# Kernel optimization log

Measured on AMD Instinct MI355X. Metric: run time of the kernel, lower is better.

The kernel has to match this reference:

```python
import jax, jax.numpy as jnp
import numpy as np

N_EMBD = 1024
N_HEAD = 16
D_HEAD = N_EMBD // N_HEAD
B, T = 4, 2048


def _layernorm(x, g, b, eps=1e-5):
    mu = jnp.mean(x, axis=-1, keepdims=True)
    var = jnp.var(x, axis=-1, keepdims=True)
    return (x - mu) * jax.lax.rsqrt(var + eps) * g + b


def setup_inputs() -> dict:
    key = jax.random.key(0)
    ks = jax.random.split(key, 16)
    C = N_EMBD
    s = 0.02
    return {
        "x": jax.random.normal(ks[0], (B, T, C), jnp.float32),
        "ln1_g": jnp.ones((C,), jnp.float32),
        "ln1_b": jnp.zeros((C,), jnp.float32),
        "Wq": jax.random.normal(ks[1], (C, C), jnp.float32) * s,
        "bq": jnp.zeros((C,), jnp.float32),
        "Wk": jax.random.normal(ks[2], (C, C), jnp.float32) * s,
        "bk": jnp.zeros((C,), jnp.float32),
        "Wv": jax.random.normal(ks[3], (C, C), jnp.float32) * s,
        "bv": jnp.zeros((C,), jnp.float32),
        "Wo": jax.random.normal(ks[4], (C, C), jnp.float32) * s,
        "bo": jnp.zeros((C,), jnp.float32),
        "ln2_g": jnp.ones((C,), jnp.float32),
        "ln2_b": jnp.zeros((C,), jnp.float32),
        "W1": jax.random.normal(ks[5], (C, 4 * C), jnp.float32) * s,
        "b1": jnp.zeros((4 * C,), jnp.float32),
        "W2": jax.random.normal(ks[6], (4 * C, C), jnp.float32) * s,
        "b2": jnp.zeros((C,), jnp.float32),
    }


def reference(x, ln1_g, ln1_b, Wq, bq, Wk, bk, Wv, bv, Wo, bo,
              ln2_g, ln2_b, W1, b1, W2, b2):
    Bx, Tx, C = x.shape
    H, D = N_HEAD, D_HEAD

    # --- attention (pre-LN) ---
    h = _layernorm(x, ln1_g, ln1_b)
    q = (h @ Wq + bq).reshape(Bx, Tx, H, D)
    k = (h @ Wk + bk).reshape(Bx, Tx, H, D)
    v = (h @ Wv + bv).reshape(Bx, Tx, H, D)
    att = jnp.einsum("bqhd,bkhd->bhqk", q, k) * (1.0 / jnp.sqrt(jnp.float32(D)))
    causal = jnp.tril(jnp.ones((Tx, Tx), bool))
    att = jnp.where(causal, att, -jnp.inf)
    att = jax.nn.softmax(att, axis=-1)
    y = jnp.einsum("bhqk,bkhd->bqhd", att, v).reshape(Bx, Tx, C)
    x = x + (y @ Wo + bo)

    # --- MLP (pre-LN), exact GELU as in torch F.gelu default ---
    h2 = _layernorm(x, ln2_g, ln2_b)
    m = jax.nn.gelu(h2 @ W1 + b1, approximate=False)
    x = x + (m @ W2 + b2)
    return x
```

## Files before the change

### kernel.cpp

```cpp
#include <hip/hip_runtime.h>
#include <hip/hip_bf16.h>
#include <math.h>

#define C_EMBD 1024
#define T_SEQ  2048
#define BATCH  4
#define NHEAD  16
#define DHEAD  64

typedef __attribute__((ext_vector_type(8))) short bf16x8;
typedef __attribute__((ext_vector_type(4))) float floatx4;

static __device__ __forceinline__ floatx4 mfma16(bf16x8 a, bf16x8 b, floatx4 c) {
    return __builtin_amdgcn_mfma_f32_16x16x32_bf16(a, b, c, 0, 0, 0);
}

static __device__ __forceinline__ void gl2lds16(const void* g, void* l) {
    __builtin_amdgcn_global_load_lds(
        (const __attribute__((address_space(1))) void*)g,
        (__attribute__((address_space(3))) void*)l, 16, 0, 0);
}

__global__ __launch_bounds__(256) void transpose_cvt(
        const float* __restrict__ W, __hip_bfloat16* __restrict__ Wt, int K, int N) {
    __shared__ float tile[32][33];
    const int tid = threadIdx.x;
    const int n0 = blockIdx.x * 32, k0 = blockIdx.y * 32;
    const int r = tid >> 3, c4 = (tid & 7) * 4;
    float4 v = *(const float4*)&W[(size_t)(k0 + r) * N + n0 + c4];
    tile[r][c4 + 0] = v.x; tile[r][c4 + 1] = v.y;
    tile[r][c4 + 2] = v.z; tile[r][c4 + 3] = v.w;
    __syncthreads();
    __align__(8) __hip_bfloat16 ob[4];
    ob[0] = __float2bfloat16(tile[c4 + 0][r]);
    ob[1] = __float2bfloat16(tile[c4 + 1][r]);
    ob[2] = __float2bfloat16(tile[c4 + 2][r]);
    ob[3] = __float2bfloat16(tile[c4 + 3][r]);
    *(short4*)&Wt[(size_t)(n0 + r) * K + k0 + c4] = *(short4*)ob;
}

__global__ __launch_bounds__(256) void ln_bf16(
        const float* __restrict__ x, const float* __restrict__ g,
        const float* __restrict__ b, __hip_bfloat16* __restrict__ out) {
    const int row = blockIdx.x, tid = threadIdx.x;
    const float4 v = ((const float4*)(x + (size_t)row * C_EMBD))[tid];
    float s  = v.x + v.y + v.z + v.w;
    float sq = v.x * v.x + v.y * v.y + v.z * v.z + v.w * v.w;
    #pragma unroll
    for (int off = 1; off < 64; off <<= 1) {
        s  += __shfl_xor(s, off);
        sq += __shfl_xor(sq, off);
    }
    __shared__ float ps[4], pq[4];
    if ((tid & 63) == 0) { ps[tid >> 6] = s; pq[tid >> 6] = sq; }
    __syncthreads();
    s  = ps[0] + ps[1] + ps[2] + ps[3];
    sq = pq[0] + pq[1] + pq[2] + pq[3];
    const float mu   = s * (1.0f / C_EMBD);
    const float var  = sq * (1.0f / C_EMBD) - mu * mu;
    const float rstd = rsqrtf(var + 1e-5f);
    const float4 gv = ((const float4*)g)[tid];
    const float4 bv = ((const float4*)b)[tid];
    __align__(8) __hip_bfloat16 ob[4];
    ob[0] = __float2bfloat16((v.x - mu) * rstd * gv.x + bv.x);
    ob[1] = __float2bfloat16((v.y - mu) * rstd * gv.y + bv.y);
    ob[2] = __float2bfloat16((v.z - mu) * rstd * gv.z + bv.z);
    ob[3] = __float2bfloat16((v.w - mu) * rstd * gv.w + bv.w);
    *(short4*)&out[(size_t)row * C_EMBD + tid * 4] = *(short4*)ob;
}

template <int EP>
__global__ __launch_bounds__(256, 2) void gemm_bt(
        const __hip_bfloat16* __restrict__ A, const __hip_bfloat16* __restrict__ Bt,
        int M, int N, int K,
        const float* __restrict__ ba, const float* __restrict__ bb, const float* __restrict__ bc,
        __hip_bfloat16* __restrict__ o0, __hip_bfloat16* __restrict__ o1,
        __hip_bfloat16* __restrict__ o2, float* __restrict__ of,
        const float* __restrict__ resid) {
    __shared__ __align__(16) __hip_bfloat16 As[128 * 32];
    __shared__ __align__(16) __hip_bfloat16 Bs[128 * 32];
    const int tid  = threadIdx.x;
    const int n0   = blockIdx.x * 128;
    const int m0   = blockIdx.y * 128;
    const int wave = tid >> 6, lane = tid & 63;
    const int l15  = lane & 15, quad = lane >> 4;
    const int wm   = (wave & 1) * 64, wn = (wave >> 1) * 64;
    const int c0   = wave * 2;
    const int sr   = lane >> 2;
    const int sc   = (lane & 3) * 8;

    const floatx4 z4 = {0.f, 0.f, 0.f, 0.f};
    floatx4 acc[4][4];
    #pragma unroll
    for (int i = 0; i < 4; i++)
        #pragma unroll
        for (int j = 0; j < 4; j++) acc[i][j] = z4;

    for (int k0 = 0; k0 < K; k0 += 32) {
        __syncthreads();
        gl2lds16(&A[(m0 + c0 * 16 + sr) * K + k0 + sc],       &As[c0 * 512]);
        gl2lds16(&A[(m0 + (c0 + 1) * 16 + sr) * K + k0 + sc], &As[(c0 + 1) * 512]);
        gl2lds16(&Bt[(n0 + c0 * 16 + sr) * K + k0 + sc],      &Bs[c0 * 512]);
        gl2lds16(&Bt[(n0 + (c0 + 1) * 16 + sr) * K + k0 + sc],&Bs[(c0 + 1) * 512]);
        __syncthreads();
        bf16x8 af[4], bfr[4];
        #pragma unroll
        for (int i = 0; i < 4; i++)
            af[i] = *(const bf16x8*)&As[(wm + i * 16 + l15) * 32 + quad * 8];
        #pragma unroll
        for (int j = 0; j < 4; j++)
            bfr[j] = *(const bf16x8*)&Bs[(wn + j * 16 + l15) * 32 + quad * 8];
        #pragma unroll
        for (int i = 0; i < 4; i++)
            #pragma unroll
            for (int j = 0; j < 4; j++)
                acc[i][j] = mfma16(af[i], bfr[j], acc[i][j]);
    }

    #pragma unroll
    for (int i = 0; i < 4; i++) {
        #pragma unroll
        for (int j = 0; j < 4; j++) {
            const int col = n0 + wn + j * 16 + l15;
            #pragma unroll
            for (int r = 0; r < 4; r++) {
                const int m = m0 + wm + i * 16 + quad * 4 + r;
                float val = acc[i][j][r];
                if (EP == 0) {
                    const int which = col >> 10, cn = col & 1023;
                    const float* bp = (which == 0) ? ba : (which == 1) ? bb : bc;
                    val += bp[cn];
                    const int head = cn >> 6, d = cn & 63;
                    const int bidx = m >> 11, t = m & 2047;
                    if (which == 0) {
                        val *= 0.125f;
                        o0[((bidx * NHEAD + head) * T_SEQ + t) * DHEAD + d] = __float2bfloat16(val);
                    } else if (which == 1) {
                        o1[((bidx * NHEAD + head) * T_SEQ + t) * DHEAD + d] = __float2bfloat16(val);
                    } else {
                        o2[((bidx * NHEAD + head) * DHEAD + d) * T_SEQ + t] = __float2bfloat16(val);
                    }
                } else if (EP == 1) {
                    val += ba[col];
                    of[m * N + col] = resid[m * N + col] + val;
                } else if (EP == 2) {
                    val += ba[col];
                    const float gl = 0.5f * val * (1.0f + erff(val * 0.70710678118654752f));
                    o0[m * N + col] = __float2bfloat16(gl);
                } else {
                    val += ba[col];
                    of[m * N + col] += val;
                }
            }
        }
    }
}

__global__ __launch_bounds__(256, 4) void attn_fa(
        const __hip_bfloat16* __restrict__ q, const __hip_bfloat16* __restrict__ k,
        const __hip_bfloat16* __restrict__ vt, __hip_bfloat16* __restrict__ y) {
    __shared__ __align__(16) __hip_bfloat16 pl[4][32 * 72];
    const int bh = blockIdx.y;
    const int tid = threadIdx.x;
    const int wave = tid >> 6, lane = tid & 63;
    const int l15 = lane & 15, quad = lane >> 4;
    const __hip_bfloat16* qp = q + (size_t)bh * T_SEQ * DHEAD;
    const __hip_bfloat16* kp = k + (size_t)bh * T_SEQ * DHEAD;
    const __hip_bfloat16* vp = vt + (size_t)bh * DHEAD * T_SEQ;
    const int chunk = (wave < 2) ? blockIdx.x : (31 - blockIdx.x);
    const int qw = chunk * 64 + (wave & 1) * 32;

    bf16x8 bq[2][2];
    #pragma unroll
    for (int qi = 0; qi < 2; qi++)
        #pragma unroll
        for (int h = 0; h < 2; h++)
            bq[qi][h] = *(const bf16x8*)&qp[(qw + qi * 16 + l15) * DHEAD + h * 32 + quad * 8];

    const floatx4 z4 = {0.f, 0.f, 0.f, 0.f};
    floatx4 oac[2][4];
    #pragma unroll
    for (int qi = 0; qi < 2; qi++)
        #pragma unroll
        for (int nd = 0; nd < 4; nd++) oac[qi][nd] = z4;
    float li[2] = {0.f, 0.f};

    __hip_bfloat16* myp = &pl[wave][0];

    auto body = [&](int kb, bool diag) {
        bf16x8 kf[4][2];
        #pragma unroll
        for (int nt = 0; nt < 4; nt++)
            #pragma unroll
            for (int h = 0; h < 2; h++)
                kf[nt][h] = *(const bf16x8*)&kp[(kb + nt * 16 + l15) * DHEAD + h * 32 + quad * 8];
        floatx4 sa[2][4];
        #pragma unroll
        for (int qi = 0; qi < 2; qi++)
            #pragma unroll
            for (int nt = 0; nt < 4; nt++) sa[qi][nt] = z4;
        #pragma unroll
        for (int nt = 0; nt < 4; nt++)
            #pragma unroll
            for (int h = 0; h < 2; h++) {
                sa[0][nt] = mfma16(kf[nt][h], bq[0][h], sa[0][nt]);
                sa[1][nt] = mfma16(kf[nt][h], bq[1][h], sa[1][nt]);
            }
        if (diag) {
            #pragma unroll
            for (int qi = 0; qi < 2; qi++)
                #pragma unroll
                for (int nt = 0; nt < 4; nt++)
                    #pragma unroll
                    for (int r = 0; r < 4; r++)
                        if (kb + nt * 16 + quad * 4 + r > qw + qi * 16 + l15)
                            sa[qi][nt][r] = -INFINITY;
        }
        #pragma unroll
        for (int qi = 0; qi < 2; qi++) {
            float sm = 0.f;
            #pragma unroll
            for (int nt = 0; nt < 4; nt++) {
                __align__(8) __hip_bfloat16 pk[4];
                #pragma unroll
                for (int r = 0; r < 4; r++) {
                    const float p = __expf(sa[qi][nt][r]);
                    sm += p;
                    pk[r] = __float2bfloat16(p);
                }
                *(short4*)&myp[(qi * 16 + l15) * 72 + nt * 16 + quad * 4] = *(short4*)pk;
            }
            li[qi] += sm;
        }
        asm volatile("" ::: "memory");
        bf16x8 vf[4][2];
        #pragma unroll
        for (int nd = 0; nd < 4; nd++)
            #pragma unroll
            for (int kh = 0; kh < 2; kh++)
                vf[nd][kh] = *(const bf16x8*)&vp[(nd * 16 + l15) * T_SEQ + kb + kh * 32 + quad * 8];
        asm volatile("s_waitcnt lgkmcnt(0)" ::: "memory");
        bf16x8 pf[2][2];
        #pragma unroll
        for (int qi = 0; qi < 2; qi++)
            #pragma unroll
            for (int kh = 0; kh < 2; kh++)
                pf[qi][kh] = *(const bf16x8*)&myp[(qi * 16 + l15) * 72 + kh * 32 + quad * 8];
        #pragma unroll
        for (int nd = 0; nd < 4; nd++)
            #pragma unroll
            for (int kh = 0; kh < 2; kh++) {
                oac[0][nd] = mfma16(vf[nd][kh], pf[0][kh], oac[0][nd]);
                oac[1][nd] = mfma16(vf[nd][kh], pf[1][kh], oac[1][nd]);
            }
    };

    const int nfull = chunk;
    for (int t = 0; t < nfull; t++) body(t * 64, false);
    body(nfull * 64, true);

    float inv[2];
    #pragma unroll
    for (int qi = 0; qi < 2; qi++) {
        float l = li[qi];
        l += __shfl_xor(l, 16);
        l += __shfl_xor(l, 32);
        inv[qi] = 1.0f / l;
    }
    #pragma unroll
    for (int qi = 0; qi < 2; qi++)
        #pragma unroll
        for (int nd = 0; nd < 4; nd++) {
            __align__(8) __hip_bfloat16 ok[4];
            #pragma unroll
            for (int r = 0; r < 4; r++) ok[r] = __float2bfloat16(oac[qi][nd][r] * inv[qi]);
            *(short4*)&myp[(qi * 16 + l15) * 72 + nd * 16 + quad * 4] = *(short4*)ok;
        }
    asm volatile("s_waitcnt lgkmcnt(0)" ::: "memory");
    const int b = bh >> 4, head = bh & 15;
    #pragma unroll
    for (int half = 0; half < 2; half++) {
        const int row = half * 16 + (lane >> 2);
        const int cb  = (lane & 3) * 16;
        const bf16x8 v0 = *(const bf16x8*)&myp[row * 72 + cb];
        const bf16x8 v1 = *(const bf16x8*)&myp[row * 72 + cb + 8];
        __hip_bfloat16* yr = &y[(size_t)(b * T_SEQ + qw + row) * C_EMBD + head * DHEAD + cb];
        *(bf16x8*)yr       = v0;
        *(bf16x8*)(yr + 8) = v1;
    }
}

extern "C" void kernel_launch(void* const* d_in, const int* in_sizes, int n_in,
                              void* d_out, int out_size, void* d_ws, size_t ws_size,
                              hipStream_t stream) {
    const float* x     = (const float*)d_in[0];
    const float* ln1_g = (const float*)d_in[1];
    const float* ln1_b = (const float*)d_in[2];
    const float* Wq    = (const float*)d_in[3];
    const float* bq    = (const float*)d_in[4];
    const float* Wk    = (const float*)d_in[5];
    const float* bk    = (const float*)d_in[6];
    const float* Wv    = (const float*)d_in[7];
    const float* bv    = (const float*)d_in[8];
    const float* Wo    = (const float*)d_in[9];
    const float* bo    = (const float*)d_in[10];
    const float* ln2_g = (const float*)d_in[11];
    const float* ln2_b = (const float*)d_in[12];
    const float* W1    = (const float*)d_in[13];
    const float* b1    = (const float*)d_in[14];
    const float* W2    = (const float*)d_in[15];
    const float* b2    = (const float*)d_in[16];
    float* out = (float*)d_out;

    char* ws = (char*)d_ws;
    __hip_bfloat16* wqkvt = (__hip_bfloat16*)(ws);
    __hip_bfloat16* wot   = (__hip_bfloat16*)(ws + 6291456);
    __hip_bfloat16* w1t   = (__hip_bfloat16*)(ws + 8388608);
    __hip_bfloat16* w2t   = (__hip_bfloat16*)(ws + 16777216);
    __hip_bfloat16* hbuf  = (__hip_bfloat16*)(ws + 25165824);
    __hip_bfloat16* qbuf  = (__hip_bfloat16*)(ws + 41943040);
    __hip_bfloat16* kbuf  = (__hip_bfloat16*)(ws + 58720256);
    __hip_bfloat16* vbuf  = (__hip_bfloat16*)(ws + 75497472);
    __hip_bfloat16* ybuf  = (__hip_bfloat16*)(ws + 92274688);
    __hip_bfloat16* mbuf  = (__hip_bfloat16*)(ws + 41943040);

    transpose_cvt<<<dim3(32, 32), 256, 0, stream>>>(Wq, wqkvt, 1024, 1024);
    transpose_cvt<<<dim3(32, 32), 256, 0, stream>>>(Wk, wqkvt + 1024 * 1024, 1024, 1024);
    transpose_cvt<<<dim3(32, 32), 256, 0, stream>>>(Wv, wqkvt + 2048 * 1024, 1024, 1024);
    transpose_cvt<<<dim3(32, 32), 256, 0, stream>>>(Wo, wot, 1024, 1024);
    transpose_cvt<<<dim3(128, 32), 256, 0, stream>>>(W1, w1t, 1024, 4096);
    transpose_cvt<<<dim3(32, 128), 256, 0, stream>>>(W2, w2t, 4096, 1024);

    ln_bf16<<<8192, 256, 0, stream>>>(x, ln1_g, ln1_b, hbuf);

    gemm_bt<0><<<dim3(24, 64), 256, 0, stream>>>(hbuf, wqkvt, 8192, 3072, 1024,
        bq, bk, bv, qbuf, kbuf, vbuf, nullptr, nullptr);

    attn_fa<<<dim3(16, 64), 256, 0, stream>>>(qbuf, kbuf, vbuf, ybuf);

    gemm_bt<1><<<dim3(8, 64), 256, 0, stream>>>(ybuf, wot, 8192, 1024, 1024,
        bo, nullptr, nullptr, nullptr, nullptr, nullptr, out, x);

    ln_bf16<<<8192, 256, 0, stream>>>(out, ln2_g, ln2_b, hbuf);

    gemm_bt<2><<<dim3(32, 64), 256, 0, stream>>>(hbuf, w1t, 8192, 4096, 1024,
        b1, nullptr, nullptr, mbuf, nullptr, nullptr, nullptr, nullptr);

    gemm_bt<3><<<dim3(8, 64), 256, 0, stream>>>(mbuf, w2t, 8192, 1024, 4096,
        b2, nullptr, nullptr, nullptr, nullptr, nullptr, out, nullptr);
}
```

Before: 610.6 us.

## Rebalance causal attention waves, remap blocks per XCD, and use exp2 softmax

Each wave now processes one 16-row query tile from a low chunk and one from the mirrored high chunk, so every wave in a block carries the same causal workload. The low-tile QK and PV MFMAs are skipped once past its diagonal. Blocks are linearly remapped so that the blocks on each XCD share the same batch-heads, aiming for better L2 reuse of K and V. The Q scale folds in log2(e) so the kernel can use the hardware exp2 instruction instead of __expf, and the extra branching adds some control overhead.

Measured after the change: 802.6 us. 1.31x slower.

```diff
diff --git a/kernel.cpp b/kernel.cpp
--- a/kernel.cpp
+++ b/kernel.cpp
@@ -10,6 +10,12 @@
 
 typedef __attribute__((ext_vector_type(8))) short bf16x8;
 typedef __attribute__((ext_vector_type(4))) float floatx4;
+
+#if __has_builtin(__builtin_amdgcn_exp2f)
+#define EXP2F __builtin_amdgcn_exp2f
+#else
+#define EXP2F exp2f
+#endif
 
 static __device__ __forceinline__ floatx4 mfma16(bf16x8 a, bf16x8 b, floatx4 c) {
     return __builtin_amdgcn_mfma_f32_16x16x32_bf16(a, b, c, 0, 0, 0);
@@ -133,7 +139,7 @@
                     const int head = cn >> 6, d = cn & 63;
                     const int bidx = m >> 11, t = m & 2047;
                     if (which == 0) {
-                        val *= 0.125f;
+                        val *= 0.18033688011112042f;
                         o0[((bidx * NHEAD + head) * T_SEQ + t) * DHEAD + d] = __float2bfloat16(val);
                     } else if (which == 1) {
                         o1[((bidx * NHEAD + head) * T_SEQ + t) * DHEAD + d] = __float2bfloat16(val);
@@ -160,22 +166,30 @@
         const __hip_bfloat16* __restrict__ q, const __hip_bfloat16* __restrict__ k,
         const __hip_bfloat16* __restrict__ vt, __hip_bfloat16* __restrict__ y) {
     __shared__ __align__(16) __hip_bfloat16 pl[4][32 * 72];
-    const int bh = blockIdx.y;
     const int tid = threadIdx.x;
     const int wave = tid >> 6, lane = tid & 63;
     const int l15 = lane & 15, quad = lane >> 4;
+
+    const int lin  = blockIdx.x + 16 * blockIdx.y;
+    const int xcd  = lin & 7;
+    const int slot = lin >> 3;
+    const int bh   = xcd * 8 + (slot >> 4);
+    const int c    = slot & 15;
+    const int hc   = 31 - c;
+
     const __hip_bfloat16* qp = q + (size_t)bh * T_SEQ * DHEAD;
     const __hip_bfloat16* kp = k + (size_t)bh * T_SEQ * DHEAD;
     const __hip_bfloat16* vp = vt + (size_t)bh * DHEAD * T_SEQ;
-    const int chunk = (wave < 2) ? blockIdx.x : (31 - blockIdx.x);
-    const int qw = chunk * 64 + (wave & 1) * 32;
+
+    const int qlo = c  * 64 + wave * 16;
+    const int qhi = hc * 64 + wave * 16;
 
     bf16x8 bq[2][2];
     #pragma unroll
-    for (int qi = 0; qi < 2; qi++)
-        #pragma unroll
-        for (int h = 0; h < 2; h++)
-            bq[qi][h] = *(const bf16x8*)&qp[(qw + qi * 16 + l15) * DHEAD + h * 32 + quad * 8];
+    for (int h = 0; h < 2; h++) {
+        bq[0][h] = *(const bf16x8*)&qp[(qlo + l15) * DHEAD + h * 32 + quad * 8];
+        bq[1][h] = *(const bf16x8*)&qp[(qhi + l15) * DHEAD + h * 32 + quad * 8];
+    }
 
     const floatx4 z4 = {0.f, 0.f, 0.f, 0.f};
     floatx4 oac[2][4];
@@ -187,7 +201,7 @@
 
     __hip_bfloat16* myp = &pl[wave][0];
 
-    auto body = [&](int kb, bool diag) {
+    auto body = [&](int kb, bool act0, bool m0, bool m1) {
         bf16x8 kf[4][2];
         #pragma unroll
         for (int nt = 0; nt < 4; nt++)
@@ -202,35 +216,60 @@
         #pragma unroll
         for (int nt = 0; nt < 4; nt++)
             #pragma unroll
-            for (int h = 0; h < 2; h++) {
-                sa[0][nt] = mfma16(kf[nt][h], bq[0][h], sa[0][nt]);
+            for (int h = 0; h < 2; h++)
                 sa[1][nt] = mfma16(kf[nt][h], bq[1][h], sa[1][nt]);
-            }
-        if (diag) {
-            #pragma unroll
-            for (int qi = 0; qi < 2; qi++)
-                #pragma unroll
-                for (int nt = 0; nt < 4; nt++)
-                    #pragma unroll
-                    for (int r = 0; r < 4; r++)
-                        if (kb + nt * 16 + quad * 4 + r > qw + qi * 16 + l15)
-                            sa[qi][nt][r] = -INFINITY;
-        }
-        #pragma unroll
-        for (int qi = 0; qi < 2; qi++) {
+        if (act0) {
+            #pragma unroll
+            for (int nt = 0; nt < 4; nt++)
+                #pragma unroll
+                for (int h = 0; h < 2; h++)
+                    sa[0][nt] = mfma16(kf[nt][h], bq[0][h], sa[0][nt]);
+        }
+        if (m1) {
+            #pragma unroll
+            for (int nt = 0; nt < 4; nt++)
+                #pragma unroll
+                for (int r = 0; r < 4; r++)
+                    if (kb + nt * 16 + quad * 4 + r > qhi + l15)
+                        sa[1][nt][r] = -INFINITY;
+        }
+        if (m0) {
+            #pragma unroll
+            for (int nt = 0; nt < 4; nt++)
+                #pragma unroll
+                for (int r = 0; r < 4; r++)
+                    if (kb + nt * 16 + quad * 4 + r > qlo + l15)
+                        sa[0][nt][r] = -INFINITY;
+        }
+        {
             float sm = 0.f;
             #pragma unroll
             for (int nt = 0; nt < 4; nt++) {
                 __align__(8) __hip_bfloat16 pk[4];
                 #pragma unroll
                 for (int r = 0; r < 4; r++) {
-                    const float p = __expf(sa[qi][nt][r]);
+                    const float p = EXP2F(sa[1][nt][r]);
                     sm += p;
                     pk[r] = __float2bfloat16(p);
                 }
-                *(short4*)&myp[(qi * 16 + l15) * 72 + nt * 16 + quad * 4] = *(short4*)pk;
+                *(short4*)&myp[(16 + l15) * 72 + nt * 16 + quad * 4] = *(short4*)pk;
             }
-            li[qi] += sm;
+            li[1] += sm;
+        }
+        if (act0) {
+            float sm = 0.f;
+            #pragma unroll
+            for (int nt = 0; nt < 4; nt++) {
+                __align__(8) __hip_bfloat16 pk[4];
+                #pragma unroll
+                for (int r = 0; r < 4; r++) {
+                    const float p = EXP2F(sa[0][nt][r]);
+                    sm += p;
+                    pk[r] = __float2bfloat16(p);
+                }
+                *(short4*)&myp[(l15) * 72 + nt * 16 + quad * 4] = *(short4*)pk;
+            }
+            li[0] += sm;
         }
         asm volatile("" ::: "memory");
         bf16x8 vf[4][2];
@@ -240,24 +279,33 @@
             for (int kh = 0; kh < 2; kh++)
                 vf[nd][kh] = *(const bf16x8*)&vp[(nd * 16 + l15) * T_SEQ + kb + kh * 32 + quad * 8];
         asm volatile("s_waitcnt lgkmcnt(0)" ::: "memory");
-        bf16x8 pf[2][2];
-        #pragma unroll
-        for (int qi = 0; qi < 2; qi++)
+        bf16x8 pf1[2];
+        #pragma unroll
+        for (int kh = 0; kh < 2; kh++)
+            pf1[kh] = *(const bf16x8*)&myp[(16 + l15) * 72 + kh * 32 + quad * 8];
+        if (act0) {
+            bf16x8 pf0[2];
             #pragma unroll
             for (int kh = 0; kh < 2; kh++)
-                pf[qi][kh] = *(const bf16x8*)&myp[(qi * 16 + l15) * 72 + kh * 32 + quad * 8];
-        #pragma unroll
-        for (int nd = 0; nd < 4; nd++)
-            #pragma unroll
-            for (int kh = 0; kh < 2; kh++) {
-                oac[0][nd] = mfma16(vf[nd][kh], pf[0][kh], oac[0][nd]);
-                oac[1][nd] = mfma16(vf[nd][kh], pf[1][kh], oac[1][nd]);
-            }
+                pf0[kh] = *(const bf16x8*)&myp[(l15) * 72 + kh * 32 + quad * 8];
+            #pragma unroll
+            for (int nd = 0; nd < 4; nd++)
+                #pragma unroll
+                for (int kh = 0; kh < 2; kh++) {
+                    oac[0][nd] = mfma16(vf[nd][kh], pf0[kh], oac[0][nd]);
+                    oac[1][nd] = mfma16(vf[nd][kh], pf1[kh], oac[1][nd]);
+                }
+        } else {
+            #pragma unroll
+            for (int nd = 0; nd < 4; nd++)
+                #pragma unroll
+                for (int kh = 0; kh < 2; kh++)
+                    oac[1][nd] = mfma16(vf[nd][kh], pf1[kh], oac[1][nd]);
+        }
     };
 
-    const int nfull = chunk;
-    for (int t = 0; t < nfull; t++) body(t * 64, false);
-    body(nfull * 64, true);
+    for (int t = 0; t < hc; t++) body(t * 64, t <= c, t == c, false);
+    body(hc * 64, false, false, true);
 
     float inv[2];
     #pragma unroll
@@ -280,11 +328,12 @@
     const int b = bh >> 4, head = bh & 15;
     #pragma unroll
     for (int half = 0; half < 2; half++) {
-        const int row = half * 16 + (lane >> 2);
+        const int row = lane >> 2;
         const int cb  = (lane & 3) * 16;
-        const bf16x8 v0 = *(const bf16x8*)&myp[row * 72 + cb];
-        const bf16x8 v1 = *(const bf16x8*)&myp[row * 72 + cb + 8];
-        __hip_bfloat16* yr = &y[(size_t)(b * T_SEQ + qw + row) * C_EMBD + head * DHEAD + cb];
+        const bf16x8 v0 = *(const bf16x8*)&myp[(half * 16 + row) * 72 + cb];
+        const bf16x8 v1 = *(const bf16x8*)&myp[(half * 16 + row) * 72 + cb + 8];
+        const int qr = (half ? qhi : qlo) + row;
+        __hip_bfloat16* yr = &y[(size_t)(b * T_SEQ + qr) * C_EMBD + head * DHEAD + cb];
         *(bf16x8*)yr       = v0;
         *(bf16x8*)(yr + 8) = v1;
     }
```

## Remap attention blocks per XCD, split waves to 16 rows, use exp2

Applied to the files above, without the earlier changes.

The flash-attention kernel now assigns all four waves of a block to the same query chunk, 16 rows each. Each block processes a chunk and its mirror chunk one after the other, instead of pairing them across waves. Block indices are remapped so that all chunks of one batch-head land on the same XCD, which should improve L2 reuse of K and V. The softmax scale is folded together with log2(e) into Q so the exponential can use the native exp2 instruction. In exchange, each wave now reuses its K/V fragments over half as many query rows, raising load traffic per MFMA.

New measurement: 729.4 us. 19.5% more time.

```diff
diff --git a/kernel.cpp b/kernel.cpp
--- a/kernel.cpp
+++ b/kernel.cpp
@@ -10,6 +10,12 @@
 
 typedef __attribute__((ext_vector_type(8))) short bf16x8;
 typedef __attribute__((ext_vector_type(4))) float floatx4;
+
+#if __has_builtin(__builtin_amdgcn_exp2f)
+#define EXP2F __builtin_amdgcn_exp2f
+#else
+#define EXP2F exp2f
+#endif
 
 static __device__ __forceinline__ floatx4 mfma16(bf16x8 a, bf16x8 b, floatx4 c) {
     return __builtin_amdgcn_mfma_f32_16x16x32_bf16(a, b, c, 0, 0, 0);
@@ -133,7 +139,7 @@
                     const int head = cn >> 6, d = cn & 63;
                     const int bidx = m >> 11, t = m & 2047;
                     if (which == 0) {
-                        val *= 0.125f;
+                        val *= 0.18033688011112042f;
                         o0[((bidx * NHEAD + head) * T_SEQ + t) * DHEAD + d] = __float2bfloat16(val);
                     } else if (which == 1) {
                         o1[((bidx * NHEAD + head) * T_SEQ + t) * DHEAD + d] = __float2bfloat16(val);
@@ -159,135 +165,119 @@
 __global__ __launch_bounds__(256, 4) void attn_fa(
         const __hip_bfloat16* __restrict__ q, const __hip_bfloat16* __restrict__ k,
         const __hip_bfloat16* __restrict__ vt, __hip_bfloat16* __restrict__ y) {
-    __shared__ __align__(16) __hip_bfloat16 pl[4][32 * 72];
-    const int bh = blockIdx.y;
+    __shared__ __align__(16) __hip_bfloat16 pl[4][16 * 72];
     const int tid = threadIdx.x;
     const int wave = tid >> 6, lane = tid & 63;
     const int l15 = lane & 15, quad = lane >> 4;
+
+    const int lin  = blockIdx.x + 16 * blockIdx.y;
+    const int xcd  = lin & 7;
+    const int slot = lin >> 3;
+    const int bh   = xcd * 8 + (slot >> 4);
+    const int c    = slot & 15;
+    const int hc   = 31 - c;
+
     const __hip_bfloat16* qp = q + (size_t)bh * T_SEQ * DHEAD;
     const __hip_bfloat16* kp = k + (size_t)bh * T_SEQ * DHEAD;
     const __hip_bfloat16* vp = vt + (size_t)bh * DHEAD * T_SEQ;
-    const int chunk = (wave < 2) ? blockIdx.x : (31 - blockIdx.x);
-    const int qw = chunk * 64 + (wave & 1) * 32;
-
-    bf16x8 bq[2][2];
-    #pragma unroll
-    for (int qi = 0; qi < 2; qi++)
+    __hip_bfloat16* myp = &pl[wave][0];
+    const int b = bh >> 4, head = bh & 15;
+
+    auto segment = [&](const int cc) {
+        const int qw = cc * 64 + wave * 16;
+
+        bf16x8 bq[2];
         #pragma unroll
         for (int h = 0; h < 2; h++)
-            bq[qi][h] = *(const bf16x8*)&qp[(qw + qi * 16 + l15) * DHEAD + h * 32 + quad * 8];
-
-    const floatx4 z4 = {0.f, 0.f, 0.f, 0.f};
-    floatx4 oac[2][4];
-    #pragma unroll
-    for (int qi = 0; qi < 2; qi++)
-        #pragma unroll
-        for (int nd = 0; nd < 4; nd++) oac[qi][nd] = z4;
-    float li[2] = {0.f, 0.f};
-
-    __hip_bfloat16* myp = &pl[wave][0];
-
-    auto body = [&](int kb, bool diag) {
-        bf16x8 kf[4][2];
-        #pragma unroll
-        for (int nt = 0; nt < 4; nt++)
-            #pragma unroll
-            for (int h = 0; h < 2; h++)
-                kf[nt][h] = *(const bf16x8*)&kp[(kb + nt * 16 + l15) * DHEAD + h * 32 + quad * 8];
-        floatx4 sa[2][4];
-        #pragma unroll
-        for (int qi = 0; qi < 2; qi++)
-            #pragma unroll
-            for (int nt = 0; nt < 4; nt++) sa[qi][nt] = z4;
-        #pragma unroll
-        for (int nt = 0; nt < 4; nt++)
-            #pragma unroll
-            for (int h = 0; h < 2; h++) {
-                sa[0][nt] = mfma16(kf[nt][h], bq[0][h], sa[0][nt]);
-                sa[1][nt] = mfma16(kf[nt][h], bq[1][h], sa[1][nt]);
-            }
-        if (diag) {
-            #pragma unroll
-            for (int qi = 0; qi < 2; qi++)
+            bq[h] = *(const bf16x8*)&qp[(qw + l15) * DHEAD + h * 32 + quad * 8];
+
+        const floatx4 z4 = {0.f, 0.f, 0.f, 0.f};
+        floatx4 oac[4];
+        #pragma unroll
+        for (int nd = 0; nd < 4; nd++) oac[nd] = z4;
+        float li = 0.f;
+
+        auto body = [&](int kb, bool diag) {
+            bf16x8 kf[4][2];
+            #pragma unroll
+            for (int nt = 0; nt < 4; nt++)
+                #pragma unroll
+                for (int h = 0; h < 2; h++)
+                    kf[nt][h] = *(const bf16x8*)&kp[(kb + nt * 16 + l15) * DHEAD + h * 32 + quad * 8];
+            floatx4 sa[4];
+            #pragma unroll
+            for (int nt = 0; nt < 4; nt++) sa[nt] = z4;
+            #pragma unroll
+            for (int nt = 0; nt < 4; nt++)
+                #pragma unroll
+                for (int h = 0; h < 2; h++)
+                    sa[nt] = mfma16(kf[nt][h], bq[h], sa[nt]);
+            if (diag) {
                 #pragma unroll
                 for (int nt = 0; nt < 4; nt++)
                     #pragma unroll
                     for (int r = 0; r < 4; r++)
-                        if (kb + nt * 16 + quad * 4 + r > qw + qi * 16 + l15)
-                            sa[qi][nt][r] = -INFINITY;
-        }
-        #pragma unroll
-        for (int qi = 0; qi < 2; qi++) {
+                        if (kb + nt * 16 + quad * 4 + r > qw + l15)
+                            sa[nt][r] = -INFINITY;
+            }
             float sm = 0.f;
             #pragma unroll
             for (int nt = 0; nt < 4; nt++) {
                 __align__(8) __hip_bfloat16 pk[4];
                 #pragma unroll
                 for (int r = 0; r < 4; r++) {
-                    const float p = __expf(sa[qi][nt][r]);
+                    const float p = EXP2F(sa[nt][r]);
                     sm += p;
                     pk[r] = __float2bfloat16(p);
                 }
-                *(short4*)&myp[(qi * 16 + l15) * 72 + nt * 16 + quad * 4] = *(short4*)pk;
+                *(short4*)&myp[l15 * 72 + nt * 16 + quad * 4] = *(short4*)pk;
             }
-            li[qi] += sm;
-        }
-        asm volatile("" ::: "memory");
-        bf16x8 vf[4][2];
-        #pragma unroll
-        for (int nd = 0; nd < 4; nd++)
+            li += sm;
+            asm volatile("" ::: "memory");
+            bf16x8 vf[4][2];
+            #pragma unroll
+            for (int nd = 0; nd < 4; nd++)
+                #pragma unroll
+                for (int kh = 0; kh < 2; kh++)
+                    vf[nd][kh] = *(const bf16x8*)&vp[(nd * 16 + l15) * T_SEQ + kb + kh * 32 + quad * 8];
+            asm volatile("s_waitcnt lgkmcnt(0)" ::: "memory");
+            bf16x8 pf[2];
             #pragma unroll
             for (int kh = 0; kh < 2; kh++)
-                vf[nd][kh] = *(const bf16x8*)&vp[(nd * 16 + l15) * T_SEQ + kb + kh * 32 + quad * 8];
-        asm volatile("s_waitcnt lgkmcnt(0)" ::: "memory");
-        bf16x8 pf[2][2];
-        #pragma unroll
-        for (int qi = 0; qi < 2; qi++)
-            #pragma unroll
-            for (int kh = 0; kh < 2; kh++)
-                pf[qi][kh] = *(const bf16x8*)&myp[(qi * 16 + l15) * 72 + kh * 32 + quad * 8];
-        #pragma unroll
-        for (int nd = 0; nd < 4; nd++)
-            #pragma unroll
-            for (int kh = 0; kh < 2; kh++) {
-                oac[0][nd] = mfma16(vf[nd][kh], pf[0][kh], oac[0][nd]);
-                oac[1][nd] = mfma16(vf[nd][kh], pf[1][kh], oac[1][nd]);
-            }
-    };
-
-    const int nfull = chunk;
-    for (int t = 0; t < nfull; t++) body(t * 64, false);
-    body(nfull * 64, true);
-
-    float inv[2];
-    #pragma unroll
-    for (int qi = 0; qi < 2; qi++) {
-        float l = li[qi];
+                pf[kh] = *(const bf16x8*)&myp[l15 * 72 + kh * 32 + quad * 8];
+            #pragma unroll
+            for (int nd = 0; nd < 4; nd++)
+                #pragma unroll
+                for (int kh = 0; kh < 2; kh++)
+                    oac[nd] = mfma16(vf[nd][kh], pf[kh], oac[nd]);
+        };
+
+        for (int t = 0; t < cc; t++) body(t * 64, false);
+        body(cc * 64, true);
+
+        float l = li;
         l += __shfl_xor(l, 16);
         l += __shfl_xor(l, 32);
-        inv[qi] = 1.0f / l;
-    }
-    #pragma unroll
-    for (int qi = 0; qi < 2; qi++)
+        const float inv = 1.0f / l;
         #pragma unroll
         for (int nd = 0; nd < 4; nd++) {
             __align__(8) __hip_bfloat16 ok[4];
             #pragma unroll
-            for (int r = 0; r < 4; r++) ok[r] = __float2bfloat16(oac[qi][nd][r] * inv[qi]);
-            *(short4*)&myp[(qi * 16 + l15) * 72 + nd * 16 + quad * 4] = *(short4*)ok;
+            for (int r = 0; r < 4; r++) ok[r] = __float2bfloat16(oac[nd][r] * inv);
+            *(short4*)&myp[l15 * 72 + nd * 16 + quad * 4] = *(short4*)ok;
         }
-    asm volatile("s_waitcnt lgkmcnt(0)" ::: "memory");
-    const int b = bh >> 4, head = bh & 15;
-    #pragma unroll
-    for (int half = 0; half < 2; half++) {
-        const int row = half * 16 + (lane >> 2);
+        asm volatile("s_waitcnt lgkmcnt(0)" ::: "memory");
+        const int row = lane >> 2;
         const int cb  = (lane & 3) * 16;
         const bf16x8 v0 = *(const bf16x8*)&myp[row * 72 + cb];
         const bf16x8 v1 = *(const bf16x8*)&myp[row * 72 + cb + 8];
         __hip_bfloat16* yr = &y[(size_t)(b * T_SEQ + qw + row) * C_EMBD + head * DHEAD + cb];
         *(bf16x8*)yr       = v0;
         *(bf16x8*)(yr + 8) = v1;
-    }
+    };
+
+    segment(c);
+    segment(hc);
 }
 
 extern "C" void kernel_launch(void* const* d_in, const int* in_sizes, int n_in,
```

## Restructure attention into 2-wave blocks with register prefetch, XCD-aware mapping, exp2

Applied to the files above, without the earlier changes.

The attention kernel now uses 128-thread blocks. Each wave processes two 32-row query segments in sequence, one early chunk and its mirrored late chunk, which balances the causal work inside each wave. K and V fragments for the next key block are prefetched into registers during the current block's MFMAs. A 1D grid is remapped so that blocks sharing a batch-head land on the same XCD, which should improve L2 reuse of K/V. The Q scale folds in log2(e) so the softmax can use the hardware exp2 instruction instead of __expf. The risks are higher register pressure from double-buffered fragments and lower per-block occupancy.

New measurement: 620.2 us. About the same (+1.6%).

```diff
diff --git a/kernel.cpp b/kernel.cpp
--- a/kernel.cpp
+++ b/kernel.cpp
@@ -10,6 +10,12 @@
 
 typedef __attribute__((ext_vector_type(8))) short bf16x8;
 typedef __attribute__((ext_vector_type(4))) float floatx4;
+
+#if __has_builtin(__builtin_amdgcn_exp2f)
+#define EXP2F __builtin_amdgcn_exp2f
+#else
+#define EXP2F exp2f
+#endif
 
 static __device__ __forceinline__ floatx4 mfma16(bf16x8 a, bf16x8 b, floatx4 c) {
     return __builtin_amdgcn_mfma_f32_16x16x32_bf16(a, b, c, 0, 0, 0);
@@ -133,7 +139,7 @@
                     const int head = cn >> 6, d = cn & 63;
                     const int bidx = m >> 11, t = m & 2047;
                     if (which == 0) {
-                        val *= 0.125f;
+                        val *= 0.18033688011112042f;
                         o0[((bidx * NHEAD + head) * T_SEQ + t) * DHEAD + d] = __float2bfloat16(val);
                     } else if (which == 1) {
                         o1[((bidx * NHEAD + head) * T_SEQ + t) * DHEAD + d] = __float2bfloat16(val);
@@ -156,138 +162,161 @@
     }
 }
 
-__global__ __launch_bounds__(256, 4) void attn_fa(
+__global__ __launch_bounds__(128, 2) void attn_fa(
         const __hip_bfloat16* __restrict__ q, const __hip_bfloat16* __restrict__ k,
         const __hip_bfloat16* __restrict__ vt, __hip_bfloat16* __restrict__ y) {
-    __shared__ __align__(16) __hip_bfloat16 pl[4][32 * 72];
-    const int bh = blockIdx.y;
+    __shared__ __align__(16) __hip_bfloat16 pl[2][32 * 72];
     const int tid = threadIdx.x;
     const int wave = tid >> 6, lane = tid & 63;
     const int l15 = lane & 15, quad = lane >> 4;
+
+    const int lin  = blockIdx.x;
+    const int xcd  = lin & 7;
+    const int slot = lin >> 3;
+    const int bh   = xcd * 8 + (slot >> 4);
+    const int c    = slot & 15;
+    const int hc   = 31 - c;
+
     const __hip_bfloat16* qp = q + (size_t)bh * T_SEQ * DHEAD;
     const __hip_bfloat16* kp = k + (size_t)bh * T_SEQ * DHEAD;
     const __hip_bfloat16* vp = vt + (size_t)bh * DHEAD * T_SEQ;
-    const int chunk = (wave < 2) ? blockIdx.x : (31 - blockIdx.x);
-    const int qw = chunk * 64 + (wave & 1) * 32;
-
-    bf16x8 bq[2][2];
-    #pragma unroll
-    for (int qi = 0; qi < 2; qi++)
-        #pragma unroll
-        for (int h = 0; h < 2; h++)
-            bq[qi][h] = *(const bf16x8*)&qp[(qw + qi * 16 + l15) * DHEAD + h * 32 + quad * 8];
-
+    __hip_bfloat16* myp = &pl[wave][0];
+    const int b = bh >> 4, head = bh & 15;
     const floatx4 z4 = {0.f, 0.f, 0.f, 0.f};
-    floatx4 oac[2][4];
-    #pragma unroll
-    for (int qi = 0; qi < 2; qi++)
-        #pragma unroll
-        for (int nd = 0; nd < 4; nd++) oac[qi][nd] = z4;
-    float li[2] = {0.f, 0.f};
-
-    __hip_bfloat16* myp = &pl[wave][0];
-
-    auto body = [&](int kb, bool diag) {
-        bf16x8 kf[4][2];
+
+    auto segment = [&](const int qw) {
+        const int cc = qw >> 6;
+
+        bf16x8 bq[2][2];
+        #pragma unroll
+        for (int qi = 0; qi < 2; qi++)
+            #pragma unroll
+            for (int h = 0; h < 2; h++)
+                bq[qi][h] = *(const bf16x8*)&qp[(qw + qi * 16 + l15) * DHEAD + h * 32 + quad * 8];
+
+        floatx4 oac[2][4];
+        #pragma unroll
+        for (int qi = 0; qi < 2; qi++)
+            #pragma unroll
+            for (int nd = 0; nd < 4; nd++) oac[qi][nd] = z4;
+        float li[2] = {0.f, 0.f};
+
+        bf16x8 kf[4][2], vf[4][2];
         #pragma unroll
         for (int nt = 0; nt < 4; nt++)
             #pragma unroll
             for (int h = 0; h < 2; h++)
-                kf[nt][h] = *(const bf16x8*)&kp[(kb + nt * 16 + l15) * DHEAD + h * 32 + quad * 8];
-        floatx4 sa[2][4];
-        #pragma unroll
-        for (int qi = 0; qi < 2; qi++)
-            #pragma unroll
-            for (int nt = 0; nt < 4; nt++) sa[qi][nt] = z4;
-        #pragma unroll
-        for (int nt = 0; nt < 4; nt++)
-            #pragma unroll
-            for (int h = 0; h < 2; h++) {
-                sa[0][nt] = mfma16(kf[nt][h], bq[0][h], sa[0][nt]);
-                sa[1][nt] = mfma16(kf[nt][h], bq[1][h], sa[1][nt]);
-            }
-        if (diag) {
+                kf[nt][h] = *(const bf16x8*)&kp[(nt * 16 + l15) * DHEAD + h * 32 + quad * 8];
+        #pragma unroll
+        for (int nd = 0; nd < 4; nd++)
+            #pragma unroll
+            for (int kh = 0; kh < 2; kh++)
+                vf[nd][kh] = *(const bf16x8*)&vp[(nd * 16 + l15) * T_SEQ + kh * 32 + quad * 8];
+
+        auto body = [&](const int kb, const bool last) {
+            floatx4 sa[2][4];
             #pragma unroll
             for (int qi = 0; qi < 2; qi++)
+                #pragma unroll
+                for (int nt = 0; nt < 4; nt++) sa[qi][nt] = z4;
+            #pragma unroll
+            for (int nt = 0; nt < 4; nt++)
+                #pragma unroll
+                for (int h = 0; h < 2; h++) {
+                    sa[0][nt] = mfma16(kf[nt][h], bq[0][h], sa[0][nt]);
+                    sa[1][nt] = mfma16(kf[nt][h], bq[1][h], sa[1][nt]);
+                }
+            if (!last) {
                 #pragma unroll
                 for (int nt = 0; nt < 4; nt++)
                     #pragma unroll
-                    for (int r = 0; r < 4; r++)
-                        if (kb + nt * 16 + quad * 4 + r > qw + qi * 16 + l15)
-                            sa[qi][nt][r] = -INFINITY;
+                    for (int h = 0; h < 2; h++)
+                        kf[nt][h] = *(const bf16x8*)&kp[(kb + 64 + nt * 16 + l15) * DHEAD + h * 32 + quad * 8];
+            }
+            if (last) {
+                #pragma unroll
+                for (int qi = 0; qi < 2; qi++)
+                    #pragma unroll
+                    for (int nt = 0; nt < 4; nt++)
+                        #pragma unroll
+                        for (int r = 0; r < 4; r++)
+                            if (kb + nt * 16 + quad * 4 + r > qw + qi * 16 + l15)
+                                sa[qi][nt][r] = -INFINITY;
+            }
+            #pragma unroll
+            for (int qi = 0; qi < 2; qi++) {
+                float sm = 0.f;
+                #pragma unroll
+                for (int nt = 0; nt < 4; nt++) {
+                    __align__(8) __hip_bfloat16 pk[4];
+                    #pragma unroll
+                    for (int r = 0; r < 4; r++) {
+                        const float p = EXP2F(sa[qi][nt][r]);
+                        sm += p;
+                        pk[r] = __float2bfloat16(p);
+                    }
+                    *(short4*)&myp[(qi * 16 + l15) * 72 + nt * 16 + quad * 4] = *(short4*)pk;
+                }
+                li[qi] += sm;
+            }
+            asm volatile("s_waitcnt lgkmcnt(0)" ::: "memory");
+            bf16x8 pf[2][2];
+            #pragma unroll
+            for (int qi = 0; qi < 2; qi++)
+                #pragma unroll
+                for (int kh = 0; kh < 2; kh++)
+                    pf[qi][kh] = *(const bf16x8*)&myp[(qi * 16 + l15) * 72 + kh * 32 + quad * 8];
+            #pragma unroll
+            for (int nd = 0; nd < 4; nd++)
+                #pragma unroll
+                for (int kh = 0; kh < 2; kh++) {
+                    oac[0][nd] = mfma16(vf[nd][kh], pf[0][kh], oac[0][nd]);
+                    oac[1][nd] = mfma16(vf[nd][kh], pf[1][kh], oac[1][nd]);
+                }
+            if (!last) {
+                #pragma unroll
+                for (int nd = 0; nd < 4; nd++)
+                    #pragma unroll
+                    for (int kh = 0; kh < 2; kh++)
+                        vf[nd][kh] = *(const bf16x8*)&vp[(nd * 16 + l15) * T_SEQ + kb + 64 + kh * 32 + quad * 8];
+            }
+        };
+
+        for (int t = 0; t < cc; t++) body(t * 64, false);
+        body(cc * 64, true);
+
+        float inv[2];
+        #pragma unroll
+        for (int qi = 0; qi < 2; qi++) {
+            float l = li[qi];
+            l += __shfl_xor(l, 16);
+            l += __shfl_xor(l, 32);
+            inv[qi] = 1.0f / l;
         }
         #pragma unroll
-        for (int qi = 0; qi < 2; qi++) {
-            float sm = 0.f;
-            #pragma unroll
-            for (int nt = 0; nt < 4; nt++) {
-                __align__(8) __hip_bfloat16 pk[4];
-                #pragma unroll
-                for (int r = 0; r < 4; r++) {
-                    const float p = __expf(sa[qi][nt][r]);
-                    sm += p;
-                    pk[r] = __float2bfloat16(p);
-                }
-                *(short4*)&myp[(qi * 16 + l15) * 72 + nt * 16 + quad * 4] = *(short4*)pk;
-            }
-            li[qi] += sm;
+        for (int qi = 0; qi < 2; qi++)
+            #pragma unroll
+            for (int nd = 0; nd < 4; nd++) {
+                __align__(8) __hip_bfloat16 ok[4];
+                #pragma unroll
+                for (int r = 0; r < 4; r++) ok[r] = __float2bfloat16(oac[qi][nd][r] * inv[qi]);
+                *(short4*)&myp[(qi * 16 + l15) * 72 + nd * 16 + quad * 4] = *(short4*)ok;
+            }
+        asm volatile("s_waitcnt lgkmcnt(0)" ::: "memory");
+        #pragma unroll
+        for (int half = 0; half < 2; half++) {
+            const int row = half * 16 + (lane >> 2);
+            const int cb  = (lane & 3) * 16;
+            const bf16x8 v0 = *(const bf16x8*)&myp[row * 72 + cb];
+            const bf16x8 v1 = *(const bf16x8*)&myp[row * 72 + cb + 8];
+            __hip_bfloat16* yr = &y[(size_t)(b * T_SEQ + qw + row) * C_EMBD + head * DHEAD + cb];
+            *(bf16x8*)yr       = v0;
+            *(bf16x8*)(yr + 8) = v1;
         }
-        asm volatile("" ::: "memory");
-        bf16x8 vf[4][2];
-        #pragma unroll
-        for (int nd = 0; nd < 4; nd++)
-            #pragma unroll
-            for (int kh = 0; kh < 2; kh++)
-                vf[nd][kh] = *(const bf16x8*)&vp[(nd * 16 + l15) * T_SEQ + kb + kh * 32 + quad * 8];
-        asm volatile("s_waitcnt lgkmcnt(0)" ::: "memory");
-        bf16x8 pf[2][2];
-        #pragma unroll
-        for (int qi = 0; qi < 2; qi++)
-            #pragma unroll
-            for (int kh = 0; kh < 2; kh++)
-                pf[qi][kh] = *(const bf16x8*)&myp[(qi * 16 + l15) * 72 + kh * 32 + quad * 8];
-        #pragma unroll
-        for (int nd = 0; nd < 4; nd++)
-            #pragma unroll
-            for (int kh = 0; kh < 2; kh++) {
-                oac[0][nd] = mfma16(vf[nd][kh], pf[0][kh], oac[0][nd]);
-                oac[1][nd] = mfma16(vf[nd][kh], pf[1][kh], oac[1][nd]);
-            }
     };
 
-    const int nfull = chunk;
-    for (int t = 0; t < nfull; t++) body(t * 64, false);
-    body(nfull * 64, true);
-
-    float inv[2];
-    #pragma unroll
-    for (int qi = 0; qi < 2; qi++) {
-        float l = li[qi];
-        l += __shfl_xor(l, 16);
-        l += __shfl_xor(l, 32);
-        inv[qi] = 1.0f / l;
-    }
-    #pragma unroll
-    for (int qi = 0; qi < 2; qi++)
-        #pragma unroll
-        for (int nd = 0; nd < 4; nd++) {
-            __align__(8) __hip_bfloat16 ok[4];
-            #pragma unroll
-            for (int r = 0; r < 4; r++) ok[r] = __float2bfloat16(oac[qi][nd][r] * inv[qi]);
-            *(short4*)&myp[(qi * 16 + l15) * 72 + nd * 16 + quad * 4] = *(short4*)ok;
-        }
-    asm volatile("s_waitcnt lgkmcnt(0)" ::: "memory");
-    const int b = bh >> 4, head = bh & 15;
-    #pragma unroll
-    for (int half = 0; half < 2; half++) {
-        const int row = half * 16 + (lane >> 2);
-        const int cb  = (lane & 3) * 16;
-        const bf16x8 v0 = *(const bf16x8*)&myp[row * 72 + cb];
-        const bf16x8 v1 = *(const bf16x8*)&myp[row * 72 + cb + 8];
-        __hip_bfloat16* yr = &y[(size_t)(b * T_SEQ + qw + row) * C_EMBD + head * DHEAD + cb];
-        *(bf16x8*)yr       = v0;
-        *(bf16x8*)(yr + 8) = v1;
-    }
+    segment(c * 64 + wave * 32);
+    segment(hc * 64 + wave * 32);
 }
 
 extern "C" void kernel_launch(void* const* d_in, const int* in_sizes, int n_in,
@@ -336,7 +365,7 @@
     gemm_bt<0><<<dim3(24, 64), 256, 0, stream>>>(hbuf, wqkvt, 8192, 3072, 1024,
         bq, bk, bv, qbuf, kbuf, vbuf, nullptr, nullptr);
 
-    attn_fa<<<dim3(16, 64), 256, 0, stream>>>(qbuf, kbuf, vbuf, ybuf);
+    attn_fa<<<dim3(1024), 128, 0, stream>>>(qbuf, kbuf, vbuf, ybuf);
 
     gemm_bt<1><<<dim3(8, 64), 256, 0, stream>>>(ybuf, wot, 8192, 1024, 1024,
         bo, nullptr, nullptr, nullptr, nullptr, nullptr, out, x);
```
